# Optimization experiments

Measured on AMD Instinct MI355X. Metric: run time of the kernel, lower is better.

The kernel has to match this reference:

```python
import jax, jax.numpy as jnp
import numpy as np

B, S, D = 2, 2048, 1024
H = 16
K = 21  # tisa_num_kernels
HD = D // H


def setup_inputs() -> dict:
    key = jax.random.key(0)
    ks = jax.random.split(key, 7)
    x = jax.random.normal(ks[0], (B, S, D), dtype=jnp.float32)
    # in_proj: Linear(d_model, 3*d_model, bias=False); stored as (D, 3D) for x @ w
    w_in = jax.random.normal(ks[1], (D, 3 * D), dtype=jnp.float32) * (1.0 / np.sqrt(D))
    # gate: Linear(d_model, 2*d_model) with bias
    w_gate = jax.random.normal(ks[2], (D, 2 * D), dtype=jnp.float32) * (1.0 / np.sqrt(D))
    b_gate = jnp.zeros((2 * D,), dtype=jnp.float32)
    # TISA kernel params, one set of K kernels per head
    amplitudes = jax.random.normal(ks[3], (H, K), dtype=jnp.float32) * 0.1
    sharpness = jax.random.uniform(ks[4], (H, K), dtype=jnp.float32, minval=0.05, maxval=0.3)
    max_fv, min_fv = S // 2, 5
    offsets = jax.random.uniform(ks[5], (H, K), dtype=jnp.float32, minval=-float(max_fv), maxval=float(max_fv))
    return {"x": x, "w_in": w_in, "w_gate": w_gate, "b_gate": b_gate,
            "amplitudes": amplitudes, "sharpness": sharpness, "offsets": offsets}


def _tisa_bias(amplitudes, sharpness, offsets, seq_len):
    # Translation-invariant: score depends only on relative position j - i.
    # Compute scores over the 2S-1 unique relative positions, then gather.
    rel = jnp.arange(-(seq_len - 1), seq_len, dtype=jnp.float32)  # (2S-1,)
    # (H, K, 2S-1)
    d = rel[None, None, :] - offsets[:, :, None]
    scores = amplitudes[:, :, None] * jnp.exp(-jnp.abs(sharpness)[:, :, None] * d * d)
    scores = scores.sum(axis=1)  # (H, 2S-1)
    idx = jnp.arange(seq_len)
    rel_idx = idx[None, :] - idx[:, None] + (seq_len - 1)  # (S, S) in [0, 2S-2]
    return scores[:, rel_idx]  # (H, S, S)


def reference(x, w_in, w_gate, b_gate, amplitudes, sharpness, offsets):
    b, s, d = x.shape
    proj = x @ w_in  # (B, S, 3D); layout: [k | v | q]
    k, v, q = jnp.split(proj, 3, axis=-1)

    def heads(t):  # (B, S, D) -> (B, H, S, HD)
        return t.reshape(b, s, H, HD).transpose(0, 2, 1, 3)

    q, k, v = heads(q), heads(k), heads(v)
    scale = 1.0 / jnp.sqrt(jnp.float32(HD))
    scores = jnp.einsum('bhqd,bhkd->bhqk', q, k) * scale  # (B, H, S, S)
    scores = scores + _tisa_bias(amplitudes, sharpness, offsets, s)[None]
    weights = jax.nn.softmax(scores, axis=-1)
    attn = jnp.einsum('bhqk,bhkd->bhqd', weights, v)  # (B, H, S, HD)
    out = attn.transpose(0, 2, 1, 3).reshape(b, s, d)  # (B, S, D)
    gated = out @ w_gate + b_gate  # (B, S, 2D)
    a, g = jnp.split(gated, 2, axis=-1)
    return a * jax.nn.sigmoid(g)
```

## Files before the change

### kernel.cpp

```cpp
#include <hip/hip_runtime.h>
#include <math.h>

#define B_   2
#define S_   2048
#define D_   1024
#define H_   16
#define K_   21
#define HD_  64
#define D3_  3072
#define D2_  2048
#define REL_ 4095

typedef __attribute__((ext_vector_type(8))) short bf16x8;
typedef __attribute__((ext_vector_type(8))) unsigned short u16x8;
typedef __attribute__((ext_vector_type(4))) float f32x4;

#define MFMA16(a, b, c) __builtin_amdgcn_mfma_f32_16x16x32_bf16((a), (b), (c), 0, 0, 0)

__device__ __forceinline__ unsigned short f2bf(float f) {
    union { float f; unsigned u; } v; v.f = f;
    return (unsigned short)((v.u + 0x7fffu + ((v.u >> 16) & 1u)) >> 16);
}
__device__ __forceinline__ float bf2f(unsigned short h) {
    union { unsigned u; float f; } v; v.u = ((unsigned)h) << 16;
    return v.f;
}
__device__ __forceinline__ float asf(unsigned u) {
    union { unsigned u; float f; } v; v.u = u; return v.f;
}
__device__ __forceinline__ unsigned cvtpk(float a, float b) {
    unsigned r;
    asm("v_cvt_pk_bf16_f32 %0, %1, %2" : "=v"(r) : "v"(a), "v"(b));
    return r;
}
#define SPLIT8(f, ph, pl)                                                      \
    {                                                                          \
        _Pragma("unroll")                                                      \
        for (int _t = 0; _t < 4; ++_t) ph.u[_t] = cvtpk(f[2*_t], f[2*_t+1]);   \
        _Pragma("unroll")                                                      \
        for (int _t = 0; _t < 4; ++_t) {                                       \
            float _h0 = asf(ph.u[_t] << 16);                                   \
            float _h1 = asf(ph.u[_t] & 0xffff0000u);                           \
            pl.u[_t] = cvtpk(f[2*_t] - _h0, f[2*_t+1] - _h1);                  \
        }                                                                      \
    }

__device__ __forceinline__ void gload16(const void* g, void* l) {
    __builtin_amdgcn_global_load_lds(
        (const __attribute__((address_space(1))) unsigned int*)g,
        (__attribute__((address_space(3))) unsigned int*)l, 16, 0, 0);
}

__global__ void tisa_bias_kernel(const float* __restrict__ amp,
                                 const float* __restrict__ shp,
                                 const float* __restrict__ off,
                                 float* __restrict__ bias_rel) {
    int idx = blockIdx.x * blockDim.x + threadIdx.x;
    if (idx >= H_ * REL_) return;
    int h = idx / REL_;
    int r = idx - h * REL_;
    float rel = (float)(r - (S_ - 1));
    float acc = 0.f;
    #pragma unroll
    for (int k = 0; k < K_; ++k) {
        float d = rel - off[h * K_ + k];
        acc = fmaf(amp[h * K_ + k], expf(-fabsf(shp[h * K_ + k]) * d * d), acc);
    }
    bias_rel[idx] = acc;
}

template<bool PERM>
__global__ __launch_bounds__(256) void convert_wT_kernel(
    const float* __restrict__ in, unsigned short* __restrict__ out, int Kd, int N)
{
    __shared__ float t[64][65];
    const int tid = threadIdx.x;
    const int k0 = blockIdx.y * 64;
    const int n0 = blockIdx.x * 64;
    {
        const int r  = tid >> 2;
        const int cq = (tid & 3) * 16;
        #pragma unroll
        for (int e = 0; e < 4; ++e) {
            float4 v = *(const float4*)&in[(size_t)(k0 + r) * N + n0 + cq + 4 * e];
            t[r][cq + 4 * e + 0] = v.x;
            t[r][cq + 4 * e + 1] = v.y;
            t[r][cq + 4 * e + 2] = v.z;
            t[r][cq + 4 * e + 3] = v.w;
        }
    }
    __syncthreads();
    {
        const int n  = tid >> 2;
        const int ks = (tid & 3) * 16;
        const int nkc = Kd >> 5;
        unsigned short hi[16], lo[16];
        #pragma unroll
        for (int i = 0; i < 16; ++i) {
            float v = t[ks + i][n];
            hi[i] = f2bf(v);
            lo[i] = f2bf(v - bf2f(hi[i]));
        }
        const int kg = k0 + ks;
        const int kc = kg >> 5;
        const int j0 = kg & 31;
        const int nsrc = n0 + n;
        const int dc = PERM ? ((nsrc < 1024) ? 2 * nsrc : 2 * (nsrc - 1024) + 1) : nsrc;
        unsigned short* op = out + (size_t)dc * (nkc * 64) + kc * 64;
        *(u16x8*)&op[j0]          = *(u16x8*)&hi[0];
        *(u16x8*)&op[j0 + 8]      = *(u16x8*)&hi[8];
        *(u16x8*)&op[32 + j0]     = *(u16x8*)&lo[0];
        *(u16x8*)&op[32 + j0 + 8] = *(u16x8*)&lo[8];
    }
}

template<bool ASPLIT, int EPI>
__global__ __launch_bounds__(256) void gemm_split_kernel(
    const void* Ap, const unsigned short* __restrict__ Bt,
    const float* __restrict__ bias, float* C,
    int N, int Kd, int lda, int ldc)
{
    __shared__ unsigned short Al[128 * 64];
    __shared__ unsigned short Bl[128 * 64];
    const int tid  = threadIdx.x;
    const int w    = tid >> 6;
    const int lane = tid & 63;
    const int c    = lane & 15;
    const int g    = lane >> 4;
    const int m0   = blockIdx.y * 128;
    const int n0   = blockIdx.x * 128;
    const int wrow = (w >> 1) * 64;
    const int wcol = (w & 1) * 64;
    const int nkc  = Kd >> 5;

    f32x4 acc[4][4];
    #pragma unroll
    for (int i = 0; i < 4; ++i)
        #pragma unroll
        for (int j = 0; j < 4; ++j) acc[i][j] = (f32x4){0.f, 0.f, 0.f, 0.f};

    const int srowB  = w * 8 + (lane >> 3);
    const int sslotB = lane & 7;

    for (int kc = 0; kc < nkc; ++kc) {
        if (ASPLIT) {
            #pragma unroll
            for (int i = 0; i < 4; ++i) {
                const int row = w * 32 + i * 8 + (lane >> 3);
                const char* src = (const char*)Ap + (size_t)(m0 + row) * lda
                                + kc * 128 + (((lane & 7) ^ (row & 7)) << 4);
                gload16(src, (char*)Al + w * 4096 + i * 1024);
            }
        } else {
            const int am  = tid >> 1;
            const int ah_ = tid & 1;
            const float* ap = (const float*)Ap + (size_t)(m0 + am) * lda + kc * 32 + ah_ * 16;
            float v[16];
            #pragma unroll
            for (int e = 0; e < 4; ++e)
                *(float4*)&v[4 * e] = *(const float4*)(ap + 4 * e);
            union { unsigned u[4]; bf16x8 v; } h0, l0, h1, l1;
            {
                const float* f = v;     SPLIT8(f, h0, l0);
            }
            {
                const float* f = v + 8; SPLIT8(f, h1, l1);
            }
            char* rowp = (char*)Al + am * 128;
            *(uint4*)(rowp + (((2 * ah_ + 0) ^ (am & 7)) << 4)) = *(uint4*)&h0.u[0];
            *(uint4*)(rowp + (((2 * ah_ + 1) ^ (am & 7)) << 4)) = *(uint4*)&h1.u[0];
            *(uint4*)(rowp + (((4 + 2 * ah_ + 0) ^ (am & 7)) << 4)) = *(uint4*)&l0.u[0];
            *(uint4*)(rowp + (((4 + 2 * ah_ + 1) ^ (am & 7)) << 4)) = *(uint4*)&l1.u[0];
        }
        #pragma unroll
        for (int i = 0; i < 4; ++i) {
            const int n = i * 32 + srowB;
            const unsigned short* src = Bt
                + ((size_t)(n0 + n) * nkc + kc) * 64 + ((sslotB ^ (n & 7)) << 3);
            gload16(src, (char*)Bl + i * 4096 + w * 1024);
        }
        __syncthreads();

        bf16x8 ah[4], al[4], bh[4], bl[4];
        #pragma unroll
        for (int f = 0; f < 4; ++f) {
            const int m = wrow + f * 16 + c;
            const char* rp = (const char*)Al + m * 128;
            ah[f] = *(const bf16x8*)(rp + (((g + 0) ^ (m & 7)) << 4));
            al[f] = *(const bf16x8*)(rp + (((g + 4) ^ (m & 7)) << 4));
            const int n = wcol + f * 16 + c;
            const char* rq = (const char*)Bl + n * 128;
            bh[f] = *(const bf16x8*)(rq + (((g + 0) ^ (n & 7)) << 4));
            bl[f] = *(const bf16x8*)(rq + (((g + 4) ^ (n & 7)) << 4));
        }
        #pragma unroll
        for (int mf = 0; mf < 4; ++mf)
            #pragma unroll
            for (int nf = 0; nf < 4; ++nf) {
                acc[mf][nf] = MFMA16(ah[mf], bh[nf], acc[mf][nf]);
                acc[mf][nf] = MFMA16(al[mf], bh[nf], acc[mf][nf]);
                acc[mf][nf] = MFMA16(ah[mf], bl[nf], acc[mf][nf]);
            }
        __syncthreads();
    }

    if (EPI == 1) {
        if (n0 < 1024) {
            #pragma unroll
            for (int mf = 0; mf < 4; ++mf)
                #pragma unroll
                for (int r = 0; r < 4; ++r) {
                    const int row = m0 + wrow + mf * 16 + g * 4 + r;
                    char* rowB = (char*)C + (size_t)row * 12288;
                    #pragma unroll
                    for (int nf = 0; nf < 4; ++nf) {
                        const int col = n0 + wcol + nf * 16 + c;
                        const float val = acc[mf][nf][r];
                        const unsigned short hi = f2bf(val);
                        *(unsigned short*)(rowB + 4096 + 2 * col) = hi;
                        *(unsigned short*)(rowB + 6144 + 2 * col) = f2bf(val - bf2f(hi));
                    }
                }
        } else if (n0 < 2048) {
            #pragma unroll
            for (int mf = 0; mf < 4; ++mf) {
                const int row0 = m0 + wrow + mf * 16 + g * 4;
                const int s2 = (row0 & 2047) * 2;
                const size_t ibase = (size_t)(row0 >> 11) * 1024;
                #pragma unroll
                for (int nf = 0; nf < 4; ++nf) {
                    const int d = n0 - 1024 + wcol + nf * 16 + c;
                    ushort4 hv, lv;
                    {
                        float v0 = acc[mf][nf][0], v1 = acc[mf][nf][1];
                        float v2 = acc[mf][nf][2], v3 = acc[mf][nf][3];
                        hv.x = f2bf(v0); lv.x = f2bf(v0 - bf2f(hv.x));
                        hv.y = f2bf(v1); lv.y = f2bf(v1 - bf2f(hv.y));
                        hv.z = f2bf(v2); lv.z = f2bf(v2 - bf2f(hv.z));
                        hv.w = f2bf(v3); lv.w = f2bf(v3 - bf2f(hv.w));
                    }
                    char* base = (char*)C + (ibase + d) * (size_t)24576 + s2;
                    *(ushort4*)base           = hv;
                    *(ushort4*)(base + 12288) = lv;
                }
            }
        } else {
            #pragma unroll
            for (int mf = 0; mf < 4; ++mf)
                #pragma unroll
                for (int r = 0; r < 4; ++r) {
                    const int row = m0 + wrow + mf * 16 + g * 4 + r;
                    float* cp = &C[(size_t)row * ldc + n0 + wcol + c];
                    #pragma unroll
                    for (int nf = 0; nf < 4; ++nf)
                        cp[nf * 16] = acc[mf][nf][r];
                }
        }
    } else {
        float bgs[4];
        #pragma unroll
        for (int nf = 0; nf < 4; ++nf) {
            const int jc = n0 + wcol + nf * 16 + c;
            bgs[nf] = bias[(jc & 1) ? (1024 + (jc >> 1)) : (jc >> 1)];
        }
        #pragma unroll
        for (int mf = 0; mf < 4; ++mf)
            #pragma unroll
            for (int r = 0; r < 4; ++r) {
                const int row = m0 + wrow + mf * 16 + g * 4 + r;
                #pragma unroll
                for (int nf = 0; nf < 4; ++nf) {
                    const int jc = n0 + wcol + nf * 16 + c;
                    const float val = acc[mf][nf][r] + bgs[nf];
                    const float part = __shfl_xor(val, 1);
                    if (!(c & 1))
                        C[(size_t)row * ldc + (jc >> 1)] = val / (1.f + __expf(-part));
                }
            }
    }
}

__global__ __launch_bounds__(256) void attn_mfma_kernel(
    const float* projf, char* projB, const float* __restrict__ bias_rel)
{
    __shared__ unsigned short KHI[4096], KLO[4096], VHI[4096], VLO[4096];
    __shared__ unsigned P32[4096];
    __shared__ float bias_s[128];

    const int tid  = threadIdx.x;
    const int w    = tid >> 6;
    const int lane = tid & 63;
    const int c    = lane & 15;
    const int g    = lane >> 4;
    const int bid  = blockIdx.x;
    const int xcd  = bid & 7;
    const int slot = bid >> 3;
    const int qt   = slot & 31;
    const int p    = (slot >> 5) * 8 + xcd;
    const int h    = p >> 1;
    const int b    = p & 1;
    const int qbase = qt * 64;
    const size_t rowbase = (size_t)b * S_;

    bf16x8 Qhi[2], Qlo[2];
    {
        const float* qp = projf + (rowbase + qbase + 16 * w + c) * D3_ + 2 * D_ + h * HD_;
        #pragma unroll
        for (int ck = 0; ck < 2; ++ck) {
            float q8[8];
            *(float4*)&q8[0] = *(const float4*)(qp + ck * 32 + g * 8);
            *(float4*)&q8[4] = *(const float4*)(qp + ck * 32 + g * 8 + 4);
            union { unsigned u[4]; bf16x8 v; } ph, pl;
            const float* f = q8;
            SPLIT8(f, ph, pl);
            Qhi[ck] = ph.v;
            Qlo[ck] = pl.v;
        }
    }

    f32x4 o_acc[4];
    #pragma unroll
    for (int n = 0; n < 4; ++n) o_acc[n] = (f32x4){0.f, 0.f, 0.f, 0.f};
    float m_run = -INFINITY;
    float l_run = 0.f;

    const int srow0 = w * 16 + (lane >> 3);
    const int gs0   = (lane & 7) ^ (srow0 & 7);
    uint4 rk0h, rk0l, rk1h, rk1l, rv0h, rv0l, rv1h, rv1l;
    float breg = 0.f;

#define LOADKV(ktv)                                                            \
    {                                                                          \
        const int kbase_ = (ktv) * 64;                                         \
        const char* ks0 = projB + (rowbase + kbase_ + srow0) * (size_t)12288   \
                        + 4096 + h * 128 + gs0 * 16;                           \
        const char* ks1 = ks0 + 8 * 12288;                                     \
        rk0h = *(const uint4*)ks0;  rk0l = *(const uint4*)(ks0 + 2048);        \
        rk1h = *(const uint4*)ks1;  rk1l = *(const uint4*)(ks1 + 2048);        \
        const char* vs0 = projB + (size_t)(b * 1024 + h * HD_ + srow0) * 24576 \
                        + (size_t)kbase_ * 2 + gs0 * 16;                       \
        const char* vs1 = vs0 + 8 * 24576;                                     \
        rv0h = *(const uint4*)vs0;  rv0l = *(const uint4*)(vs0 + 12288);       \
        rv1h = *(const uint4*)vs1;  rv1l = *(const uint4*)(vs1 + 12288);       \
        if (tid < 127)                                                         \
            breg = bias_rel[h * REL_ + kbase_ - qbase + tid + 1984];           \
    }

    LOADKV(0);

    for (int kt = 0; kt < S_ / 64; ++kt) {
        __syncthreads();
        {
            const int d0 = srow0 * 128 + (lane & 7) * 16;
            const int d1 = d0 + 1024;
            *(uint4*)((char*)KHI + d0) = rk0h; *(uint4*)((char*)KHI + d1) = rk1h;
            *(uint4*)((char*)KLO + d0) = rk0l; *(uint4*)((char*)KLO + d1) = rk1l;
            *(uint4*)((char*)VHI + d0) = rv0h; *(uint4*)((char*)VHI + d1) = rv1h;
            *(uint4*)((char*)VLO + d0) = rv0l; *(uint4*)((char*)VLO + d1) = rv1l;
            if (tid < 127) bias_s[tid] = breg;
        }
        if (kt + 1 < S_ / 64) LOADKV(kt + 1);
        __syncthreads();

        f32x4 sf[4];
        #pragma unroll
        for (int f = 0; f < 4; ++f) {
            f32x4 acc = (f32x4){0.f, 0.f, 0.f, 0.f};
            const int krow = f * 16 + c;
            const unsigned short* kbp = KHI + krow * 64;
            const unsigned short* klp = KLO + krow * 64;
            #pragma unroll
            for (int ck = 0; ck < 2; ++ck) {
                const int s = ((ck * 4 + g) ^ (krow & 7)) * 8;
                bf16x8 kh  = *(const bf16x8*)(kbp + s);
                bf16x8 kl8 = *(const bf16x8*)(klp + s);
                acc = MFMA16(kh, Qhi[ck], acc);
                acc = MFMA16(kl8, Qhi[ck], acc);
                acc = MFMA16(kh, Qlo[ck], acc);
            }
            sf[f] = acc;
        }

        #pragma unroll
        for (int f = 0; f < 4; ++f) {
            const int tb = 16 * f + 4 * g - 16 * w - c + 63;
            #pragma unroll
            for (int r = 0; r < 4; ++r)
                sf[f][r] = fmaf(sf[f][r], 0.125f, bias_s[tb + r]);
        }

        float pm[4];
        #pragma unroll
        for (int f = 0; f < 4; ++f)
            pm[f] = fmaxf(fmaxf(sf[f][0], sf[f][1]), fmaxf(sf[f][2], sf[f][3]));
        float mt = fmaxf(fmaxf(pm[0], pm[1]), fmaxf(pm[2], pm[3]));
        mt = fmaxf(mt, __shfl_xor(mt, 16));
        mt = fmaxf(mt, __shfl_xor(mt, 32));
        if (!__all(mt <= m_run + 8.f)) {
            const float mn = fmaxf(m_run, mt);
            const float sc = __expf(m_run - mn);
            l_run *= sc;
            m_run = mn;
            #pragma unroll
            for (int r = 0; r < 4; ++r) {
                const float scr = __shfl(sc, 20 * g + r);
                #pragma unroll
                for (int n = 0; n < 4; ++n) o_acc[n][r] *= scr;
            }
        }
        float ps[4];
        #pragma unroll
        for (int f = 0; f < 4; ++f) {
            #pragma unroll
            for (int r = 0; r < 4; ++r)
                sf[f][r] = __expf(sf[f][r] - m_run);
            ps[f] = (sf[f][0] + sf[f][1]) + (sf[f][2] + sf[f][3]);
        }
        float rs = (ps[0] + ps[1]) + (ps[2] + ps[3]);
        rs += __shfl_xor(rs, 16);
        rs += __shfl_xor(rs, 32);
        l_run += rs;

        #pragma unroll
        for (int f = 0; f < 4; ++f)
            *(f32x4*)&P32[(((16 * w + c) * 64 + 16 * f + 4 * g)) ^ ((c & 7) << 2)] = sf[f];
        asm volatile("s_waitcnt lgkmcnt(0)" ::: "memory");

        #pragma unroll
        for (int ck = 0; ck < 2; ++ck) {
            const int base = (16 * w + c) * 64 + ck * 32 + g * 8;
            const int x = (c & 7) << 2;
            uint4 w0 = *(const uint4*)&P32[base ^ x];
            uint4 w1 = *(const uint4*)&P32[(base + 4) ^ x];
            float pf[8] = {asf(w0.x), asf(w0.y), asf(w0.z), asf(w0.w),
                           asf(w1.x), asf(w1.y), asf(w1.z), asf(w1.w)};
            union { unsigned u[4]; bf16x8 v; } ph, pl;
            const float* fp = pf;
            SPLIT8(fp, ph, pl);
            #pragma unroll
            for (int n = 0; n < 4; ++n) {
                const int d = 16 * n + c;
                const int s = ((ck * 4 + g) ^ (d & 7)) * 8;
                bf16x8 vh = *(const bf16x8*)(VHI + d * 64 + s);
                bf16x8 vl = *(const bf16x8*)(VLO + d * 64 + s);
                o_acc[n] = MFMA16(ph.v, vh, o_acc[n]);
                o_acc[n] = MFMA16(pl.v, vh, o_acc[n]);
                o_acc[n] = MFMA16(ph.v, vl, o_acc[n]);
            }
        }
    }
#undef LOADKV

    const float inv = 1.f / l_run;
    #pragma unroll
    for (int r = 0; r < 4; ++r) {
        const float invr = __shfl(inv, 20 * g + r);
        unsigned short* op = (unsigned short*)(projB
            + (rowbase + qbase + 16 * w + 4 * g + r) * (size_t)12288 + 8192);
        #pragma unroll
        for (int n = 0; n < 4; ++n) {
            const float v = o_acc[n][r] * invr;
            const int col = h * HD_ + 16 * n + c;
            const int kc2 = col >> 5;
            const int j   = col & 31;
            const unsigned short hi = f2bf(v);
            op[kc2 * 64 + j]      = hi;
            op[kc2 * 64 + 32 + j] = f2bf(v - bf2f(hi));
        }
    }
}

extern "C" void kernel_launch(void* const* d_in, const int* in_sizes, int n_in,
                              void* d_out, int out_size, void* d_ws, size_t ws_size,
                              hipStream_t stream) {
    const float* x      = (const float*)d_in[0];
    const float* w_in   = (const float*)d_in[1];
    const float* w_gate = (const float*)d_in[2];
    const float* b_gate = (const float*)d_in[3];
    const float* amp    = (const float*)d_in[4];
    const float* shp    = (const float*)d_in[5];
    const float* off    = (const float*)d_in[6];
    float* outp = (float*)d_out;

    char* ws = (char*)d_ws;
    float*    proj     = (float*)ws;
    float*    bias_rel = (float*)(ws + 50331648);
    unsigned short* wT = (unsigned short*)(ws + 50331648 + 262144);

    tisa_bias_kernel<<<(H_ * REL_ + 255) / 256, 256, 0, stream>>>(amp, shp, off, bias_rel);
    convert_wT_kernel<false><<<dim3(D3_ / 64, D_ / 64), 256, 0, stream>>>(w_in, wT, D_, D3_);
    gemm_split_kernel<false, 1><<<dim3(D3_ / 128, (B_ * S_) / 128), 256, 0, stream>>>(
        x, wT, nullptr, proj, D3_, D_, D_, D3_);
    convert_wT_kernel<true><<<dim3(D2_ / 64, D_ / 64), 256, 0, stream>>>(w_gate, wT, D_, D2_);
    attn_mfma_kernel<<<1024, 256, 0, stream>>>(proj, ws, bias_rel);
    gemm_split_kernel<true, 2><<<dim3(D2_ / 128, (B_ * S_) / 128), 256, 0, stream>>>(
        ws + 8192, wT, b_gate, outp, D2_, D_, 12288, D_);
}
```

Before: 321.6 us.

## Use 128-query attention tiles with 8 waves and bf16 P staging

The attention kernel now runs 512-thread blocks that each cover 128 queries instead of 64. Each K/V tile loaded into shared memory is therefore reused by twice as many waves, and each thread loads half as much. Probabilities are split into bf16 hi/lo halves in registers before the shared-memory round trip, instead of storing fp32 and splitting after the reload. s_setprio is raised around the MFMA sections to favour matrix work. The cost is fewer blocks (512), which may reduce occupancy and latency hiding, plus a larger bias window per tile.

```diff
diff --git a/kernel.cpp b/kernel.cpp
--- a/kernel.cpp
+++ b/kernel.cpp
@@ -280,12 +280,12 @@
     }
 }
 
-__global__ __launch_bounds__(256) void attn_mfma_kernel(
+__global__ __launch_bounds__(512) void attn_mfma_kernel(
     const float* projf, char* projB, const float* __restrict__ bias_rel)
 {
     __shared__ unsigned short KHI[4096], KLO[4096], VHI[4096], VLO[4096];
-    __shared__ unsigned P32[4096];
-    __shared__ float bias_s[128];
+    __shared__ unsigned short PHI[4096], PLO[4096];
+    __shared__ float bias_s[192];
 
     const int tid  = threadIdx.x;
     const int w    = tid >> 6;
@@ -295,16 +295,17 @@
     const int bid  = blockIdx.x;
     const int xcd  = bid & 7;
     const int slot = bid >> 3;
-    const int qt   = slot & 31;
-    const int p    = (slot >> 5) * 8 + xcd;
+    const int qt   = slot & 15;
+    const int p    = (slot >> 4) * 8 + xcd;
     const int h    = p >> 1;
     const int b    = p & 1;
-    const int qbase = qt * 64;
+    const int qbase = qt * 128;
     const size_t rowbase = (size_t)b * S_;
+    const int q    = 16 * w + c;
 
     bf16x8 Qhi[2], Qlo[2];
     {
-        const float* qp = projf + (rowbase + qbase + 16 * w + c) * D3_ + 2 * D_ + h * HD_;
+        const float* qp = projf + (rowbase + qbase + q) * D3_ + 2 * D_ + h * HD_;
         #pragma unroll
         for (int ck = 0; ck < 2; ++ck) {
             float q8[8];
@@ -324,26 +325,22 @@
     float m_run = -INFINITY;
     float l_run = 0.f;
 
-    const int srow0 = w * 16 + (lane >> 3);
-    const int gs0   = (lane & 7) ^ (srow0 & 7);
-    uint4 rk0h, rk0l, rk1h, rk1l, rv0h, rv0l, rv1h, rv1l;
+    const int srow = tid >> 3;
+    const int gsl  = (tid & 7) ^ (srow & 7);
+    uint4 rkh, rkl, rvh, rvl;
     float breg = 0.f;
 
 #define LOADKV(ktv)                                                            \
     {                                                                          \
         const int kbase_ = (ktv) * 64;                                         \
-        const char* ks0 = projB + (rowbase + kbase_ + srow0) * (size_t)12288   \
-                        + 4096 + h * 128 + gs0 * 16;                           \
-        const char* ks1 = ks0 + 8 * 12288;                                     \
-        rk0h = *(const uint4*)ks0;  rk0l = *(const uint4*)(ks0 + 2048);        \
-        rk1h = *(const uint4*)ks1;  rk1l = *(const uint4*)(ks1 + 2048);        \
-        const char* vs0 = projB + (size_t)(b * 1024 + h * HD_ + srow0) * 24576 \
-                        + (size_t)kbase_ * 2 + gs0 * 16;                       \
-        const char* vs1 = vs0 + 8 * 24576;                                     \
-        rv0h = *(const uint4*)vs0;  rv0l = *(const uint4*)(vs0 + 12288);       \
-        rv1h = *(const uint4*)vs1;  rv1l = *(const uint4*)(vs1 + 12288);       \
-        if (tid < 127)                                                         \
-            breg = bias_rel[h * REL_ + kbase_ - qbase + tid + 1984];           \
+        const char* ks = projB + (rowbase + kbase_ + srow) * (size_t)12288     \
+                       + 4096 + h * 128 + gsl * 16;                            \
+        rkh = *(const uint4*)ks;  rkl = *(const uint4*)(ks + 2048);            \
+        const char* vs = projB + (size_t)(b * 1024 + h * HD_ + srow) * 24576   \
+                       + (size_t)kbase_ * 2 + gsl * 16;                        \
+        rvh = *(const uint4*)vs;  rvl = *(const uint4*)(vs + 12288);           \
+        if (tid < 191)                                                         \
+            breg = bias_rel[h * REL_ + kbase_ - qbase + 1920 + tid];           \
     }
 
     LOADKV(0);
@@ -351,18 +348,18 @@
     for (int kt = 0; kt < S_ / 64; ++kt) {
         __syncthreads();
         {
-            const int d0 = srow0 * 128 + (lane & 7) * 16;
-            const int d1 = d0 + 1024;
-            *(uint4*)((char*)KHI + d0) = rk0h; *(uint4*)((char*)KHI + d1) = rk1h;
-            *(uint4*)((char*)KLO + d0) = rk0l; *(uint4*)((char*)KLO + d1) = rk1l;
-            *(uint4*)((char*)VHI + d0) = rv0h; *(uint4*)((char*)VHI + d1) = rv1h;
-            *(uint4*)((char*)VLO + d0) = rv0l; *(uint4*)((char*)VLO + d1) = rv1l;
-            if (tid < 127) bias_s[tid] = breg;
+            const int d = srow * 128 + (tid & 7) * 16;
+            *(uint4*)((char*)KHI + d) = rkh;
+            *(uint4*)((char*)KLO + d) = rkl;
+            *(uint4*)((char*)VHI + d) = rvh;
+            *(uint4*)((char*)VLO + d) = rvl;
+            if (tid < 191) bias_s[tid] = breg;
         }
         if (kt + 1 < S_ / 64) LOADKV(kt + 1);
         __syncthreads();
 
         f32x4 sf[4];
+        __builtin_amdgcn_s_setprio(1);
         #pragma unroll
         for (int f = 0; f < 4; ++f) {
             f32x4 acc = (f32x4){0.f, 0.f, 0.f, 0.f};
@@ -380,10 +377,11 @@
             }
             sf[f] = acc;
         }
+        __builtin_amdgcn_s_setprio(0);
 
         #pragma unroll
         for (int f = 0; f < 4; ++f) {
-            const int tb = 16 * f + 4 * g - 16 * w - c + 63;
+            const int tb = 16 * f + 4 * g - q + 127;
             #pragma unroll
             for (int r = 0; r < 4; ++r)
                 sf[f][r] = fmaf(sf[f][r], 0.125f, bias_s[tb + r]);
@@ -422,31 +420,41 @@
         l_run += rs;
 
         #pragma unroll
-        for (int f = 0; f < 4; ++f)
-            *(f32x4*)&P32[(((16 * w + c) * 64 + 16 * f + 4 * g)) ^ ((c & 7) << 2)] = sf[f];
-        asm volatile("s_waitcnt lgkmcnt(0)" ::: "memory");
-
-        #pragma unroll
         for (int ck = 0; ck < 2; ++ck) {
-            const int base = (16 * w + c) * 64 + ck * 32 + g * 8;
-            const int x = (c & 7) << 2;
-            uint4 w0 = *(const uint4*)&P32[base ^ x];
-            uint4 w1 = *(const uint4*)&P32[(base + 4) ^ x];
-            float pf[8] = {asf(w0.x), asf(w0.y), asf(w0.z), asf(w0.w),
-                           asf(w1.x), asf(w1.y), asf(w1.z), asf(w1.w)};
-            union { unsigned u[4]; bf16x8 v; } ph, pl;
-            const float* fp = pf;
-            SPLIT8(fp, ph, pl);
+            #pragma unroll
+            for (int f2 = 0; f2 < 2; ++f2) {
+                const int f = 2 * ck + f2;
+                const unsigned uh0 = cvtpk(sf[f][0], sf[f][1]);
+                const unsigned uh1 = cvtpk(sf[f][2], sf[f][3]);
+                const float r0 = sf[f][0] - asf(uh0 << 16);
+                const float r1 = sf[f][1] - asf(uh0 & 0xffff0000u);
+                const float r2 = sf[f][2] - asf(uh1 << 16);
+                const float r3 = sf[f][3] - asf(uh1 & 0xffff0000u);
+                const unsigned ul0 = cvtpk(r0, r1);
+                const unsigned ul1 = cvtpk(r2, r3);
+                const int byte = q * 64
+                    + ((((2 * f2 + (g >> 1)) ^ (q & 3)) << 4) + ((g & 1) << 3));
+                uint2 vh2; vh2.x = uh0; vh2.y = uh1;
+                uint2 vl2; vl2.x = ul0; vl2.y = ul1;
+                *(uint2*)((char*)PHI + byte) = vh2;
+                *(uint2*)((char*)PLO + byte) = vl2;
+            }
+            asm volatile("s_waitcnt lgkmcnt(0)" ::: "memory");
+            const int rbyte = q * 64 + ((g ^ (q & 3)) << 4);
+            bf16x8 pah = *(const bf16x8*)((char*)PHI + rbyte);
+            bf16x8 pal = *(const bf16x8*)((char*)PLO + rbyte);
+            __builtin_amdgcn_s_setprio(1);
             #pragma unroll
             for (int n = 0; n < 4; ++n) {
                 const int d = 16 * n + c;
                 const int s = ((ck * 4 + g) ^ (d & 7)) * 8;
                 bf16x8 vh = *(const bf16x8*)(VHI + d * 64 + s);
                 bf16x8 vl = *(const bf16x8*)(VLO + d * 64 + s);
-                o_acc[n] = MFMA16(ph.v, vh, o_acc[n]);
-                o_acc[n] = MFMA16(pl.v, vh, o_acc[n]);
-                o_acc[n] = MFMA16(ph.v, vl, o_acc[n]);
-            }
+                o_acc[n] = MFMA16(pah, vh, o_acc[n]);
+                o_acc[n] = MFMA16(pal, vh, o_acc[n]);
+                o_acc[n] = MFMA16(pah, vl, o_acc[n]);
+            }
+            __builtin_amdgcn_s_setprio(0);
         }
     }
 #undef LOADKV
@@ -492,7 +500,7 @@
     gemm_split_kernel<false, 1><<<dim3(D3_ / 128, (B_ * S_) / 128), 256, 0, stream>>>(
         x, wT, nullptr, proj, D3_, D_, D_, D3_);
     convert_wT_kernel<true><<<dim3(D2_ / 64, D_ / 64), 256, 0, stream>>>(w_gate, wT, D_, D2_);
-    attn_mfma_kernel<<<1024, 256, 0, stream>>>(proj, ws, bias_rel);
+    attn_mfma_kernel<<<512, 512, 0, stream>>>(proj, ws, bias_rel);
     gemm_split_kernel<true, 2><<<dim3(D2_ / 128, (B_ * S_) / 128), 256, 0, stream>>>(
         ws + 8192, wT, b_gate, outp, D2_, D_, 12288, D_);
 }
```

Result: faster. 295.7 us (-8.1%).
